# Kernel optimization log

Hardware: AMD Instinct MI355X
Metric: run time of the kernel (lower is better)

Reference implementation:

```python
import jax, jax.numpy as jnp
import numpy as np

HALF_STEP = 0.05
NUM_V = 10  # clamp(floor(0.5/0.05), 2, 1000)
EPS = 1e-6


def _normalize(x):
    return x / (jnp.linalg.norm(x, axis=-1, keepdims=True) + EPS)


def _ragged_structure(edge_points_np):
    # Concrete (numpy) ragged-grid index structure: per-edge horizontal sample
    # counts from edge length, exclusive-cumsum offsets, repeat_interleave ids.
    sp = edge_points_np[:, 0]
    cd = edge_points_np[:, 1] - sp
    cl = np.linalg.norm(cd + EPS, axis=1)
    num_h = np.clip((cl // HALF_STEP).astype(np.int64), 2, 1000)  # [N]
    total_x = int(num_h.sum())
    begin = np.concatenate([[0], np.cumsum(num_h)[:-1]])           # roll-based exclusive cumsum
    eid_x = np.repeat(np.arange(len(num_h)), num_h)                # [total_x] edge id per x-sample
    pos_x = np.arange(total_x) - begin[eid_x]                      # dx integer position within edge
    eid = np.repeat(eid_x, NUM_V)                                  # [P] edge id per sample point
    pos_x_full = np.repeat(pos_x, NUM_V).astype(np.float32)        # coords_x integer part
    dy_idx = np.tile(np.arange(NUM_V), total_x).astype(np.float32) # coords_y integer part
    denom_full = np.repeat((num_h - 1)[eid_x], NUM_V).astype(np.float32)
    return (jnp.asarray(eid), jnp.asarray(pos_x_full), jnp.asarray(denom_full),
            jnp.asarray(dy_idx))


def _sample_img(img, uv):
    # img [1,3,H,W]; uv [P,2] in [0,1) -> bilinear sample (align_corners style)
    im = img[0]
    H, W = im.shape[1], im.shape[2]
    x = uv[:, 0] * (W - 1)
    y = uv[:, 1] * (H - 1)
    x0 = jnp.floor(x).astype(jnp.int32)
    y0 = jnp.floor(y).astype(jnp.int32)
    x1 = jnp.clip(x0 + 1, 0, W - 1)
    y1 = jnp.clip(y0 + 1, 0, H - 1)
    wx = (x - x0)[None]
    wy = (y - y0)[None]
    g = lambda yy, xx: im[:, yy, xx]  # [3,P] gather
    out = (g(y0, x0) * (1 - wx) * (1 - wy) + g(y0, x1) * wx * (1 - wy)
           + g(y1, x0) * (1 - wx) * wy + g(y1, x1) * wx * wy)
    return out.T  # [P,3]


def _forward(edge_points, intrinsic1, intrinsic2, extrinsic1, extrinsic2,
             rgb1, rgb2, eid, pos_x, denom, dy_idx):
    start = edge_points[:, 0]
    cur_dir = edge_points[:, 1] - start
    next_dir = edge_points[:, 3] - edge_points[:, 1]
    prev_dir = edge_points[:, 0] - edge_points[:, 2]
    cur_len = jnp.linalg.norm(cur_dir + EPS, axis=1)
    cur_dir = cur_dir / cur_len[:, None]
    cur_normal = _normalize(jnp.cross(cur_dir, next_dir))
    flip = cur_normal[:, 2] > 0  # dot with (0,0,1) > 0 -> flip sign
    cur_normal = jnp.where(flip[:, None], -cur_normal, cur_normal)
    cur_up = _normalize(jnp.cross(cur_normal, cur_dir))
    prev_normal = _normalize(jnp.cross(prev_dir, cur_dir))

    # ragged per-edge sample grid (repeat_interleave realized via gather on eid)
    coords_x = pos_x / denom * cur_len[eid]          # [P]
    coords_y = dy_idx / (NUM_V - 1) * 0.5            # [P]
    pts = (cur_dir[eid] * coords_x[:, None]
           + cur_up[eid] * coords_y[:, None]
           + start[eid])                              # [P,3]

    # view 1 projection + bilinear sample
    uv1 = pts @ intrinsic1.T
    uv1 = jnp.clip(uv1[:, :2] / uv1[:, 2:3], 0.0, 0.999999)
    s1 = _sample_img(rgb1, uv1)

    # view 2: K2_homog @ E2 @ inv(E1) applied to homogeneous points
    K2h = jnp.eye(4, dtype=pts.dtype).at[:3, :3].set(intrinsic2)
    T = K2h @ extrinsic2 @ jnp.linalg.inv(extrinsic1)
    ph = jnp.concatenate([pts, jnp.ones_like(pts[:, :1])], axis=1)
    uv2 = ph @ T.T
    uv2 = jnp.clip(uv2[:, :2] / uv2[:, 2:3], 0.0, 0.999999)
    s2 = _sample_img(rgb2, uv2)

    similarity_loss = jnp.mean((s1 - s2) ** 2)
    normal_loss = jnp.mean(1.0 - jnp.sum(cur_normal * prev_normal, axis=1)) / 2.0
    obs_normal = _normalize(jnp.cross(edge_points[:, 0], edge_points[:, 1]))
    snp = jnp.minimum(jnp.abs(jnp.sum(cur_up * obs_normal, axis=1)), 0.5)
    normalization_loss = jnp.mean(1.0 - snp / 0.5)
    return jnp.stack([similarity_loss, normal_loss, normalization_loss])


def setup_inputs() -> dict:
    key = jax.random.key(0)
    k0, k1, k2 = jax.random.split(key, 3)
    N, H, W = 10000, 1500, 2000
    # camera-space edge endpoints/neighbors, pushed in front of the camera
    edge_points = jax.random.normal(k0, (N, 4, 3), dtype=jnp.float32) \
        + jnp.array([0.0, 0.0, 6.0], dtype=jnp.float32)
    intrinsic1 = jnp.array([[0.3, 0.0, 0.5], [0.0, 0.3, 0.5], [0.0, 0.0, 1.0]],
                           dtype=jnp.float32)
    intrinsic2 = intrinsic1
    extrinsic1 = jnp.eye(4, dtype=jnp.float32)
    extrinsic2 = jnp.eye(4, dtype=jnp.float32).at[:3, 3].set(
        jnp.array([0.1, 0.0, 0.0], dtype=jnp.float32))
    rgb1 = jax.random.uniform(k1, (1, 3, H, W), dtype=jnp.float32)
    rgb2 = jax.random.uniform(k2, (1, 3, H, W), dtype=jnp.float32)
    return {"edge_points": edge_points, "intrinsic1": intrinsic1,
            "intrinsic2": intrinsic2, "extrinsic1": extrinsic1,
            "extrinsic2": extrinsic2, "rgb1": rgb1, "rgb2": rgb2}


def reference(edge_points, intrinsic1, intrinsic2, extrinsic1, extrinsic2,
              rgb1, rgb2):
    eid, pos_x, denom, dy_idx = _ragged_structure(np.asarray(edge_points))
    return _forward(edge_points, intrinsic1, intrinsic2, extrinsic1,
                    extrinsic2, rgb1, rgb2, eid, pos_x, denom, dy_idx)
```

## Files before the change

### kernel.cpp

```cpp
#include <hip/hip_runtime.h>
#include <math.h>

#define EPSF 1e-6f
#define NUM_V 10
#define W_IMG 2000
#define H_IMG 1500
#define HW_IMG (W_IMG * H_IMG)
#define TH_QUAD (H_IMG - 1)
#define SAMPLE_BLOCKS 2048
#define MAX_CHUNKS 80
#define ROW_MARGIN 8

__device__ __forceinline__ void cross3(const float a[3], const float b[3], float c[3]) {
    c[0] = a[1] * b[2] - a[2] * b[1];
    c[1] = a[2] * b[0] - a[0] * b[2];
    c[2] = a[0] * b[1] - a[1] * b[0];
}
__device__ __forceinline__ float dot3(const float a[3], const float b[3]) {
    return a[0] * b[0] + a[1] * b[1] + a[2] * b[2];
}
__device__ __forceinline__ float norm3(const float a[3]) {
    return sqrtf(a[0] * a[0] + a[1] * a[1] + a[2] * a[2]);
}

__device__ void do_init(const float* __restrict__ K2, const float* __restrict__ E1,
                        const float* __restrict__ E2, float* __restrict__ T) {
    double M[4][8];
    for (int i = 0; i < 4; ++i)
        for (int j = 0; j < 4; ++j) {
            M[i][j] = (double)E1[i * 4 + j];
            M[i][j + 4] = (i == j) ? 1.0 : 0.0;
        }
    for (int col = 0; col < 4; ++col) {
        int piv = col;
        double best = fabs(M[col][col]);
        for (int r = col + 1; r < 4; ++r) {
            double v = fabs(M[r][col]);
            if (v > best) { best = v; piv = r; }
        }
        if (piv != col)
            for (int j = 0; j < 8; ++j) {
                double t = M[col][j]; M[col][j] = M[piv][j]; M[piv][j] = t;
            }
        double d = M[col][col];
        for (int j = 0; j < 8; ++j) M[col][j] /= d;
        for (int r = 0; r < 4; ++r) {
            if (r == col) continue;
            double f = M[r][col];
            for (int j = 0; j < 8; ++j) M[r][j] -= f * M[col][j];
        }
    }
    double E[4][4];
    for (int i = 0; i < 4; ++i)
        for (int j = 0; j < 4; ++j) {
            double s = 0.0;
            for (int k = 0; k < 4; ++k) s += (double)E2[i * 4 + k] * M[k][j + 4];
            E[i][j] = s;
        }
    for (int i = 0; i < 4; ++i)
        for (int j = 0; j < 4; ++j) {
            double s = 0.0;
            if (i < 3) {
                for (int k = 0; k < 3; ++k) s += (double)K2[i * 3 + k] * E[k][j];
            } else {
                s = E[3][j];
            }
            T[i * 4 + j] = (float)s;
        }
}

__global__ void init_kernel(const float* __restrict__ K2, const float* __restrict__ E1,
                            const float* __restrict__ E2, float* __restrict__ T,
                            int* __restrict__ bbox) {
    if (threadIdx.x != 0) return;
    do_init(K2, E1, E2, T);
    bbox[0] = 0x7fffffff;
    bbox[1] = -0x7fffffff;
    bbox[2] = 0x7fffffff;
    bbox[3] = -0x7fffffff;
}

__global__ __launch_bounds__(256) void geom_kernel(const float* __restrict__ ep, int N,
                                                   const float* __restrict__ K1,
                                                   const float* __restrict__ T,
                                                   float4* __restrict__ geo,
                                                   int* __restrict__ nwv,
                                                   double* __restrict__ gnl,
                                                   double* __restrict__ gzl,
                                                   double* __restrict__ gcnt,
                                                   int* __restrict__ bbox) {
    const int e = blockIdx.x * 256 + threadIdx.x;
    float nl = 0.f, zl = 0.f;
    int cn = 0;
    int r1min = 0x7fffffff, r1max = -0x7fffffff;
    int r2min = 0x7fffffff, r2max = -0x7fffffff;
    if (e < N) {
        const float4* P4 = (const float4*)(ep + (size_t)e * 12);
        float4 a4 = P4[0], b4 = P4[1], c4 = P4[2];
        float p0[3] = {a4.x, a4.y, a4.z};
        float p1[3] = {a4.w, b4.x, b4.y};
        float p2[3] = {b4.z, b4.w, c4.x};
        float p3[3] = {c4.y, c4.z, c4.w};
        float cd[3] = {p1[0] - p0[0], p1[1] - p0[1], p1[2] - p0[2]};
        float nd[3] = {p3[0] - p1[0], p3[1] - p1[1], p3[2] - p1[2]};
        float pd[3] = {p0[0] - p2[0], p0[1] - p2[1], p0[2] - p2[2]};
        float ce[3] = {cd[0] + EPSF, cd[1] + EPSF, cd[2] + EPSF};
        float clen = norm3(ce);
        float dir[3] = {cd[0] / clen, cd[1] / clen, cd[2] / clen};
        float cnv[3];
        cross3(dir, nd, cnv);
        float n1 = norm3(cnv) + EPSF;
        cnv[0] /= n1; cnv[1] /= n1; cnv[2] /= n1;
        if (cnv[2] > 0.f) { cnv[0] = -cnv[0]; cnv[1] = -cnv[1]; cnv[2] = -cnv[2]; }
        float up[3];
        cross3(cnv, dir, up);
        float n2 = norm3(up) + EPSF;
        up[0] /= n2; up[1] /= n2; up[2] /= n2;
        float pn[3];
        cross3(pd, dir, pn);
        float n3 = norm3(pn) + EPSF;
        pn[0] /= n3; pn[1] /= n3; pn[2] /= n3;
        float obs[3];
        cross3(p0, p1, obs);
        float n4 = norm3(obs) + EPSF;
        obs[0] /= n4; obs[1] /= n4; obs[2] /= n4;
        int nh = (int)floorf(clen / 0.05f);
        nh = max(2, min(1000, nh));
        nl = 1.f - dot3(cnv, pn);
        float snp = fminf(fabsf(dot3(up, obs)), 0.5f);
        zl = 1.f - snp * 2.f;
        int nsamp = nh * NUM_V;
        cn = nsamp;
        geo[3 * e + 0] = make_float4(p0[0], p0[1], p0[2], clen);
        geo[3 * e + 1] = make_float4(dir[0], dir[1], dir[2], (float)(nh - 1));
        geo[3 * e + 2] = make_float4(up[0], up[1], up[2], __int_as_float(nsamp));
        nwv[e] = (nsamp + 127) / 128;

        const float k10 = K1[3], k11 = K1[4], k12 = K1[5];
        const float k20 = K1[6], k21 = K1[7], k22 = K1[8];
        const float t10 = T[4], t11 = T[5], t12 = T[6], t13 = T[7];
        const float t20 = T[8], t21 = T[9], t22 = T[10], t23 = T[11];
        float v1min = 1e9f, v1max = -1e9f, v2min = 1e9f, v2max = -1e9f;
#pragma unroll
        for (int c = 0; c < 4; ++c) {
            float cx = (c & 1) ? clen : 0.f;
            float cy = (c & 2) ? 0.5f : 0.f;
            float X = fmaf(dir[0], cx, fmaf(up[0], cy, p0[0]));
            float Y = fmaf(dir[1], cx, fmaf(up[1], cy, p0[1]));
            float Z = fmaf(dir[2], cx, fmaf(up[2], cy, p0[2]));
            float iw1 = __builtin_amdgcn_rcpf(fmaf(k20, X, fmaf(k21, Y, k22 * Z)));
            float v1 = fminf(fmaxf(fmaf(k10, X, fmaf(k11, Y, k12 * Z)) * iw1, 0.f), 0.999999f);
            float iw2 = __builtin_amdgcn_rcpf(fmaf(t20, X, fmaf(t21, Y, fmaf(t22, Z, t23))));
            float v2 = fminf(
                fmaxf(fmaf(t10, X, fmaf(t11, Y, fmaf(t12, Z, t13))) * iw2, 0.f), 0.999999f);
            v1min = fminf(v1min, v1); v1max = fmaxf(v1max, v1);
            v2min = fminf(v2min, v2); v2max = fmaxf(v2max, v2);
        }
        r1min = (int)floorf(v1min * (float)(H_IMG - 1)) - ROW_MARGIN;
        r1max = (int)floorf(v1max * (float)(H_IMG - 1)) + ROW_MARGIN;
        r2min = (int)floorf(v2min * (float)(H_IMG - 1)) - ROW_MARGIN;
        r2max = (int)floorf(v2max * (float)(H_IMG - 1)) + ROW_MARGIN;
    }
#pragma unroll
    for (int off = 32; off > 0; off >>= 1) {
        nl += __shfl_down(nl, off);
        zl += __shfl_down(zl, off);
        cn += __shfl_down(cn, off);
        r1min = min(r1min, __shfl_down(r1min, off));
        r1max = max(r1max, __shfl_down(r1max, off));
        r2min = min(r2min, __shfl_down(r2min, off));
        r2max = max(r2max, __shfl_down(r2max, off));
    }
    __shared__ int s_bb[4][4];
    const int wave = threadIdx.x >> 6;
    if ((threadIdx.x & 63) == 0) {
        const int w = blockIdx.x * 4 + wave;
        gnl[w] = (double)nl;
        gzl[w] = (double)zl;
        gcnt[w] = (double)cn;
        s_bb[wave][0] = r1min; s_bb[wave][1] = r1max;
        s_bb[wave][2] = r2min; s_bb[wave][3] = r2max;
    }
    __syncthreads();
    if (threadIdx.x == 0) {
        int m0 = min(min(s_bb[0][0], s_bb[1][0]), min(s_bb[2][0], s_bb[3][0]));
        int m1 = max(max(s_bb[0][1], s_bb[1][1]), max(s_bb[2][1], s_bb[3][1]));
        int m2 = min(min(s_bb[0][2], s_bb[1][2]), min(s_bb[2][2], s_bb[3][2]));
        int m3 = max(max(s_bb[0][3], s_bb[1][3]), max(s_bb[2][3], s_bb[3][3]));
        atomicMin(&bbox[0], m0);
        atomicMax(&bbox[1], m1);
        atomicMin(&bbox[2], m2);
        atomicMax(&bbox[3], m3);
    }
}

__global__ __launch_bounds__(256) void sched_scan_kernel(const int* __restrict__ nwv, int N,
                                                         unsigned* __restrict__ sched,
                                                         int* __restrict__ total) {
    __shared__ int s_red[256];
    const int b = blockIdx.x;
    const int tid = threadIdx.x;
    const int lo = b * 256;
    int acc = 0;
    for (int i = tid; i < lo; i += 256) acc += nwv[i];
    s_red[tid] = acc;
    __syncthreads();
    for (int off = 128; off > 0; off >>= 1) {
        if (tid < off) s_red[tid] += s_red[tid + off];
        __syncthreads();
    }
    const int base0 = s_red[0];
    __syncthreads();
    const int e = lo + tid;
    const int mine = (e < N) ? nwv[e] : 0;
    s_red[tid] = mine;
    __syncthreads();
    for (int off = 1; off < 256; off <<= 1) {
        int v = (tid >= off) ? s_red[tid - off] : 0;
        __syncthreads();
        s_red[tid] += v;
        __syncthreads();
    }
    if (e < N) {
        int basee = base0 + (s_red[tid] - mine);
        const unsigned tag = ((unsigned)e) << 8;
        for (int j = 0; j < mine; ++j) sched[basee + j] = tag | (unsigned)j;
    }
    if (b == (int)gridDim.x - 1 && tid == 255) *total = base0 + s_red[255];
}

__device__ __forceinline__ unsigned quant565(float r, float g, float b) {
    unsigned r5 = (unsigned)fmaf(r, 31.f, 0.5f);
    unsigned g6 = (unsigned)fmaf(g, 63.f, 0.5f);
    unsigned b5 = (unsigned)fmaf(b, 31.f, 0.5f);
    return (r5 << 11) | (g6 << 5) | b5;
}

__global__ __launch_bounds__(256) void repack_quad565(const float* __restrict__ rgb1,
                                                      const float* __restrict__ rgb2,
                                                      uint2* __restrict__ t1,
                                                      uint2* __restrict__ t2,
                                                      const int* __restrict__ bbox) {
    const int gpi = TH_QUAD * (W_IMG / 4);
    int t = blockIdx.x * 256 + threadIdx.x;
    if (t >= 2 * gpi) return;
    const int img = t >= gpi;
    const int g = t - img * gpi;
    const int y = g / (W_IMG / 4);
    const int bmin = max(0, bbox[img * 2]);
    const int bmax = min(TH_QUAD - 1, bbox[img * 2 + 1]);
    if (y < bmin || y > bmax) return;
    const int x = (g - y * (W_IMG / 4)) * 4;
    const float* src = img ? rgb2 : rgb1;
    uint2* dst = img ? t2 : t1;
    unsigned pk[2][5];
#pragma unroll
    for (int r = 0; r < 2; ++r) {
        const int yy = y + r;
        float px[3][5];
#pragma unroll
        for (int c = 0; c < 3; ++c) {
            const float* b = src + (size_t)c * HW_IMG + (size_t)yy * W_IMG + x;
            float4 a = *(const float4*)b;
            float e = (x + 4 < W_IMG) ? b[4] : a.w;
            px[c][0] = a.x; px[c][1] = a.y; px[c][2] = a.z; px[c][3] = a.w; px[c][4] = e;
        }
#pragma unroll
        for (int k = 0; k < 5; ++k) pk[r][k] = quant565(px[0][k], px[1][k], px[2][k]);
    }
    uint2* o = dst + (size_t)y * W_IMG + x;
    uint4 s0 = make_uint4(pk[0][0] | (pk[0][1] << 16), pk[1][0] | (pk[1][1] << 16),
                          pk[0][1] | (pk[0][2] << 16), pk[1][1] | (pk[1][2] << 16));
    uint4 s1 = make_uint4(pk[0][2] | (pk[0][3] << 16), pk[1][2] | (pk[1][3] << 16),
                          pk[0][3] | (pk[0][4] << 16), pk[1][3] | (pk[1][4] << 16));
    *(uint4*)(o + 0) = s0;
    *(uint4*)(o + 2) = s1;
}

__device__ __forceinline__ float mse565(uint2 qa, uint2 qb, float wxa, float wya, float wxb,
                                        float wyb) {
    float wa00 = (1.f - wxa) * (1.f - wya), wa01 = wxa * (1.f - wya);
    float wa10 = (1.f - wxa) * wya, wa11 = wxa * wya;
    float wb00 = (1.f - wxb) * (1.f - wyb), wb01 = wxb * (1.f - wyb);
    float wb10 = (1.f - wxb) * wyb, wb11 = wxb * wyb;
    unsigned a00 = qa.x & 0xffffu, a01 = qa.x >> 16, a10 = qa.y & 0xffffu, a11 = qa.y >> 16;
    unsigned b00 = qb.x & 0xffffu, b01 = qb.x >> 16, b10 = qb.y & 0xffffu, b11 = qb.y >> 16;
    float ra = fmaf((float)(a00 >> 11), wa00, fmaf((float)(a01 >> 11), wa01,
               fmaf((float)(a10 >> 11), wa10, (float)(a11 >> 11) * wa11)));
    float rb = fmaf((float)(b00 >> 11), wb00, fmaf((float)(b01 >> 11), wb01,
               fmaf((float)(b10 >> 11), wb10, (float)(b11 >> 11) * wb11)));
    float ga = fmaf((float)((a00 >> 5) & 63u), wa00, fmaf((float)((a01 >> 5) & 63u), wa01,
               fmaf((float)((a10 >> 5) & 63u), wa10, (float)((a11 >> 5) & 63u) * wa11)));
    float gb = fmaf((float)((b00 >> 5) & 63u), wb00, fmaf((float)((b01 >> 5) & 63u), wb01,
               fmaf((float)((b10 >> 5) & 63u), wb10, (float)((b11 >> 5) & 63u) * wb11)));
    float ba = fmaf((float)(a00 & 31u), wa00, fmaf((float)(a01 & 31u), wa01,
               fmaf((float)(a10 & 31u), wa10, (float)(a11 & 31u) * wa11)));
    float bb = fmaf((float)(b00 & 31u), wb00, fmaf((float)(b01 & 31u), wb01,
               fmaf((float)(b10 & 31u), wb10, (float)(b11 & 31u) * wb11)));
    float dr = (ra - rb) * (1.f / 31.f);
    float dg = (ga - gb) * (1.f / 63.f);
    float db = (ba - bb) * (1.f / 31.f);
    return fmaf(dr, dr, fmaf(dg, dg, db * db));
}

__global__ __launch_bounds__(256) void sample_kernel(
    const float4* __restrict__ geo, const float* __restrict__ K1, const float* __restrict__ T,
    const uint2* __restrict__ im1, const uint2* __restrict__ im2,
    const unsigned* __restrict__ sched, const int* __restrict__ total_p,
    double* __restrict__ part) {
    const int wid = blockIdx.x * 4 + (threadIdx.x >> 6);
    const int lane = threadIdx.x & 63;
    const int nw = gridDim.x * 4;
    const int total = *total_p;

    const float k00 = K1[0], k01 = K1[1], k02 = K1[2];
    const float k10 = K1[3], k11 = K1[4], k12 = K1[5];
    const float k20 = K1[6], k21 = K1[7], k22 = K1[8];
    const float t00 = T[0], t01 = T[1], t02 = T[2], t03 = T[3];
    const float t10 = T[4], t11 = T[5], t12 = T[6], t13 = T[7];
    const float t20 = T[8], t21 = T[9], t22 = T[10], t23 = T[11];

    float lsum = 0.f;
    for (int base = wid; base < total; base += 2 * nw) {
        const int idxB = base + nw;
        const bool has2 = idxB < total;
        const unsigned sA = (unsigned)__builtin_amdgcn_readfirstlane((int)sched[base]);
        const unsigned sB =
            has2 ? (unsigned)__builtin_amdgcn_readfirstlane((int)sched[idxB]) : sA;
        const int eA = (int)(sA >> 8), kA = (int)(sA & 255u);
        const int eB = (int)(sB >> 8), kB = (int)(sB & 255u);
        const float4 a0 = geo[3 * eA + 0], a1 = geo[3 * eA + 1], a2 = geo[3 * eA + 2];
        const float4 b0 = geo[3 * eB + 0], b1 = geo[3 * eB + 1], b2 = geo[3 * eB + 2];
        const int nsA = __float_as_int(a2.w), nsB = __float_as_int(b2.w);
        const float lodA = a0.w * __builtin_amdgcn_rcpf(a1.w);
        const float lodB = b0.w * __builtin_amdgcn_rcpf(b1.w);

        int off1[4], off2[4];
        float wx1[4], wy1[4], wx2[4], wy2[4];
        bool ok[4];
#pragma unroll
        for (int j = 0; j < 4; ++j) {
            const int d = j >> 1, h = j & 1;
            const float4 g0 = d ? b0 : a0;
            const float4 g1 = d ? b1 : a1;
            const float4 g2 = d ? b2 : a2;
            const int ns = d ? nsB : nsA;
            const int kk = d ? kB : kA;
            const float lod = d ? lodB : lodA;
            const int i = kk * 128 + h * 64 + lane;
            ok[j] = (i < ns) && (d == 0 || has2);
            const int ic = min(i, ns - 1);
            int px = ic / NUM_V;
            int dy = ic - px * NUM_V;
            float cx = (float)px * lod;
            float cy = (float)dy * (0.5f / 9.0f);
            float X = fmaf(g1.x, cx, fmaf(g2.x, cy, g0.x));
            float Y = fmaf(g1.y, cx, fmaf(g2.y, cy, g0.y));
            float Z = fmaf(g1.z, cx, fmaf(g2.z, cy, g0.z));
            float iw1 = __builtin_amdgcn_rcpf(fmaf(k20, X, fmaf(k21, Y, k22 * Z)));
            float u1 = fminf(fmaxf(fmaf(k00, X, fmaf(k01, Y, k02 * Z)) * iw1, 0.f), 0.999999f);
            float v1 = fminf(fmaxf(fmaf(k10, X, fmaf(k11, Y, k12 * Z)) * iw1, 0.f), 0.999999f);
            float iw2 = __builtin_amdgcn_rcpf(fmaf(t20, X, fmaf(t21, Y, fmaf(t22, Z, t23))));
            float u2 = fminf(
                fmaxf(fmaf(t00, X, fmaf(t01, Y, fmaf(t02, Z, t03))) * iw2, 0.f), 0.999999f);
            float v2 = fminf(
                fmaxf(fmaf(t10, X, fmaf(t11, Y, fmaf(t12, Z, t13))) * iw2, 0.f), 0.999999f);
            float xa = u1 * (float)(W_IMG - 1), ya = v1 * (float)(H_IMG - 1);
            float xb = u2 * (float)(W_IMG - 1), yb = v2 * (float)(H_IMG - 1);
            float fxa = floorf(xa), fya = floorf(ya), fxb = floorf(xb), fyb = floorf(yb);
            off1[j] = (int)fya * W_IMG + (int)fxa;
            off2[j] = (int)fyb * W_IMG + (int)fxb;
            wx1[j] = xa - fxa; wy1[j] = ya - fya;
            wx2[j] = xb - fxb; wy2[j] = yb - fyb;
        }
        uint2 q1[4], q2[4];
#pragma unroll
        for (int j = 0; j < 4; ++j) q1[j] = im1[off1[j]];
#pragma unroll
        for (int j = 0; j < 4; ++j) q2[j] = im2[off2[j]];
#pragma unroll
        for (int j = 0; j < 4; ++j) {
            float v = mse565(q1[j], q2[j], wx1[j], wy1[j], wx2[j], wy2[j]);
            lsum += ok[j] ? v : 0.f;
        }
    }
    double dsum = (double)lsum;
#pragma unroll
    for (int off = 32; off > 0; off >>= 1) dsum += __shfl_down(dsum, off);
    if (lane == 0) part[wid] = dsum;
}

__global__ __launch_bounds__(256) void finalize_kernel(const double* __restrict__ part, int NP,
                                                       const double* __restrict__ gnl,
                                                       const double* __restrict__ gzl,
                                                       const double* __restrict__ gcnt, int N,
                                                       int NW, float* __restrict__ out) {
    __shared__ double s_s[4], s_a[4], s_b[4], s_c[4];
    double s = 0.0, a = 0.0, b = 0.0, c = 0.0;
    for (int i = threadIdx.x; i < NP; i += 256) s += part[i];
    for (int i = threadIdx.x; i < NW; i += 256) {
        a += gnl[i];
        b += gzl[i];
        c += gcnt[i];
    }
#pragma unroll
    for (int off = 32; off > 0; off >>= 1) {
        s += __shfl_down(s, off);
        a += __shfl_down(a, off);
        b += __shfl_down(b, off);
        c += __shfl_down(c, off);
    }
    const int wave = threadIdx.x >> 6;
    if ((threadIdx.x & 63) == 0) {
        s_s[wave] = s; s_a[wave] = a; s_b[wave] = b; s_c[wave] = c;
    }
    __syncthreads();
    if (threadIdx.x == 0) {
        double S = s_s[0] + s_s[1] + s_s[2] + s_s[3];
        double A = s_a[0] + s_a[1] + s_a[2] + s_a[3];
        double B = s_b[0] + s_b[1] + s_b[2] + s_b[3];
        double C = s_c[0] + s_c[1] + s_c[2] + s_c[3];
        out[0] = (float)(S / (C * 3.0));
        out[1] = (float)(A / (double)N * 0.5);
        out[2] = (float)(B / (double)N);
    }
}

extern "C" void kernel_launch(void* const* d_in, const int* in_sizes, int n_in, void* d_out,
                              int out_size, void* d_ws, size_t ws_size, hipStream_t stream) {
    const float* ep = (const float*)d_in[0];
    const float* K1 = (const float*)d_in[1];
    const float* K2 = (const float*)d_in[2];
    const float* E1 = (const float*)d_in[3];
    const float* E2 = (const float*)d_in[4];
    const float* rgb1 = (const float*)d_in[5];
    const float* rgb2 = (const float*)d_in[6];
    float* out = (float*)d_out;
    const int N = in_sizes[0] / 12;

    const int GB = (N + 255) / 256;
    const int NW = GB * 4;
    const int NPART = SAMPLE_BLOCKS * 4;

    char* p = (char*)d_ws;
    auto align256 = [](char* q) { return (char*)(((size_t)q + 255) & ~(size_t)255); };
    float* T = (float*)p;                 p += 256;
    int* total = (int*)p;                 p += 128;
    int* bbox = (int*)p;                  p += 128;
    float4* geo = (float4*)p;             p += (size_t)3 * N * sizeof(float4);
    p = align256(p);
    int* nwv = (int*)p;                   p += (size_t)N * sizeof(int);
    p = align256(p);
    double* part = (double*)p;            p += (size_t)NPART * sizeof(double);
    double* gnl = (double*)p;             p += (size_t)NW * sizeof(double);
    double* gzl = (double*)p;             p += (size_t)NW * sizeof(double);
    double* gcnt = (double*)p;            p += (size_t)NW * sizeof(double);
    p = align256(p);
    unsigned* sched = (unsigned*)p;       p += (size_t)N * MAX_CHUNKS * sizeof(unsigned);
    p = align256(p);
    uint2* img1 = (uint2*)p;
    uint2* img2 = img1 + (size_t)TH_QUAD * W_IMG;

    init_kernel<<<1, 64, 0, stream>>>(K2, E1, E2, T, bbox);
    geom_kernel<<<GB, 256, 0, stream>>>(ep, N, K1, T, geo, nwv, gnl, gzl, gcnt, bbox);
    sched_scan_kernel<<<GB, 256, 0, stream>>>(nwv, N, sched, total);
    const int rp_threads = 2 * TH_QUAD * (W_IMG / 4);
    repack_quad565<<<(rp_threads + 255) / 256, 256, 0, stream>>>(rgb1, rgb2, img1, img2, bbox);
    sample_kernel<<<SAMPLE_BLOCKS, 256, 0, stream>>>(geo, K1, T, img1, img2, sched, total, part);
    finalize_kernel<<<1, 256, 0, stream>>>(part, NPART, gnl, gzl, gcnt, N, NW, out);
}
```

Baseline: 178.6 us.

## Fuse prep stages into one kernel, atomic scheduling, drop bbox culling

Merges the init, geometry, schedule-scan and image-repack kernels into a single prep kernel. The prefix-scan schedule is replaced by an atomic cursor, and the finalize kernel is replaced by atomic accumulation with a last-block-done reduction. Sample waves now take contiguous chunk ranges instead of a strided pair loop. This cuts launch count and serialization between stages, but it removes the bbox-based row culling, so the repack now converts every image row, and the atomic schedule order is nondeterministic.

```diff
diff --git a/kernel.cpp b/kernel.cpp
--- a/kernel.cpp
+++ b/kernel.cpp
@@ -8,8 +8,18 @@
 #define HW_IMG (W_IMG * H_IMG)
 #define TH_QUAD (H_IMG - 1)
 #define SAMPLE_BLOCKS 2048
+#define NW_WAVES (SAMPLE_BLOCKS * 4)
 #define MAX_CHUNKS 80
-#define ROW_MARGIN 8
+
+struct Ctrl {
+    int cursor;
+    int done;
+    int pad0, pad1;
+    double accS;
+    double accNL;
+    double accZL;
+    double accC;
+};
 
 __device__ __forceinline__ void cross3(const float a[3], const float b[3], float c[3]) {
     c[0] = a[1] * b[2] - a[2] * b[1];
@@ -23,210 +33,51 @@
     return sqrtf(a[0] * a[0] + a[1] * a[1] + a[2] * a[2]);
 }
 
-__device__ void do_init(const float* __restrict__ K2, const float* __restrict__ E1,
-                        const float* __restrict__ E2, float* __restrict__ T) {
-    double M[4][8];
+__device__ void make_T(const float* __restrict__ K2, const float* __restrict__ E1,
+                       const float* __restrict__ E2, float* __restrict__ T) {
+    float M[4][8];
     for (int i = 0; i < 4; ++i)
         for (int j = 0; j < 4; ++j) {
-            M[i][j] = (double)E1[i * 4 + j];
-            M[i][j + 4] = (i == j) ? 1.0 : 0.0;
+            M[i][j] = E1[i * 4 + j];
+            M[i][j + 4] = (i == j) ? 1.f : 0.f;
         }
     for (int col = 0; col < 4; ++col) {
         int piv = col;
-        double best = fabs(M[col][col]);
+        float best = fabsf(M[col][col]);
         for (int r = col + 1; r < 4; ++r) {
-            double v = fabs(M[r][col]);
+            float v = fabsf(M[r][col]);
             if (v > best) { best = v; piv = r; }
         }
         if (piv != col)
             for (int j = 0; j < 8; ++j) {
-                double t = M[col][j]; M[col][j] = M[piv][j]; M[piv][j] = t;
+                float t = M[col][j]; M[col][j] = M[piv][j]; M[piv][j] = t;
             }
-        double d = M[col][col];
-        for (int j = 0; j < 8; ++j) M[col][j] /= d;
+        float d = 1.f / M[col][col];
+        for (int j = 0; j < 8; ++j) M[col][j] *= d;
         for (int r = 0; r < 4; ++r) {
             if (r == col) continue;
-            double f = M[r][col];
+            float f = M[r][col];
             for (int j = 0; j < 8; ++j) M[r][j] -= f * M[col][j];
         }
     }
-    double E[4][4];
+    float E[4][4];
     for (int i = 0; i < 4; ++i)
         for (int j = 0; j < 4; ++j) {
-            double s = 0.0;
-            for (int k = 0; k < 4; ++k) s += (double)E2[i * 4 + k] * M[k][j + 4];
+            float s = 0.f;
+            for (int k = 0; k < 4; ++k) s += E2[i * 4 + k] * M[k][j + 4];
             E[i][j] = s;
         }
     for (int i = 0; i < 4; ++i)
         for (int j = 0; j < 4; ++j) {
-            double s = 0.0;
+            float s;
             if (i < 3) {
-                for (int k = 0; k < 3; ++k) s += (double)K2[i * 3 + k] * E[k][j];
+                s = 0.f;
+                for (int k = 0; k < 3; ++k) s += K2[i * 3 + k] * E[k][j];
             } else {
                 s = E[3][j];
             }
-            T[i * 4 + j] = (float)s;
-        }
-}
-
-__global__ void init_kernel(const float* __restrict__ K2, const float* __restrict__ E1,
-                            const float* __restrict__ E2, float* __restrict__ T,
-                            int* __restrict__ bbox) {
-    if (threadIdx.x != 0) return;
-    do_init(K2, E1, E2, T);
-    bbox[0] = 0x7fffffff;
-    bbox[1] = -0x7fffffff;
-    bbox[2] = 0x7fffffff;
-    bbox[3] = -0x7fffffff;
-}
-
-__global__ __launch_bounds__(256) void geom_kernel(const float* __restrict__ ep, int N,
-                                                   const float* __restrict__ K1,
-                                                   const float* __restrict__ T,
-                                                   float4* __restrict__ geo,
-                                                   int* __restrict__ nwv,
-                                                   double* __restrict__ gnl,
-                                                   double* __restrict__ gzl,
-                                                   double* __restrict__ gcnt,
-                                                   int* __restrict__ bbox) {
-    const int e = blockIdx.x * 256 + threadIdx.x;
-    float nl = 0.f, zl = 0.f;
-    int cn = 0;
-    int r1min = 0x7fffffff, r1max = -0x7fffffff;
-    int r2min = 0x7fffffff, r2max = -0x7fffffff;
-    if (e < N) {
-        const float4* P4 = (const float4*)(ep + (size_t)e * 12);
-        float4 a4 = P4[0], b4 = P4[1], c4 = P4[2];
-        float p0[3] = {a4.x, a4.y, a4.z};
-        float p1[3] = {a4.w, b4.x, b4.y};
-        float p2[3] = {b4.z, b4.w, c4.x};
-        float p3[3] = {c4.y, c4.z, c4.w};
-        float cd[3] = {p1[0] - p0[0], p1[1] - p0[1], p1[2] - p0[2]};
-        float nd[3] = {p3[0] - p1[0], p3[1] - p1[1], p3[2] - p1[2]};
-        float pd[3] = {p0[0] - p2[0], p0[1] - p2[1], p0[2] - p2[2]};
-        float ce[3] = {cd[0] + EPSF, cd[1] + EPSF, cd[2] + EPSF};
-        float clen = norm3(ce);
-        float dir[3] = {cd[0] / clen, cd[1] / clen, cd[2] / clen};
-        float cnv[3];
-        cross3(dir, nd, cnv);
-        float n1 = norm3(cnv) + EPSF;
-        cnv[0] /= n1; cnv[1] /= n1; cnv[2] /= n1;
-        if (cnv[2] > 0.f) { cnv[0] = -cnv[0]; cnv[1] = -cnv[1]; cnv[2] = -cnv[2]; }
-        float up[3];
-        cross3(cnv, dir, up);
-        float n2 = norm3(up) + EPSF;
-        up[0] /= n2; up[1] /= n2; up[2] /= n2;
-        float pn[3];
-        cross3(pd, dir, pn);
-        float n3 = norm3(pn) + EPSF;
-        pn[0] /= n3; pn[1] /= n3; pn[2] /= n3;
-        float obs[3];
-        cross3(p0, p1, obs);
-        float n4 = norm3(obs) + EPSF;
-        obs[0] /= n4; obs[1] /= n4; obs[2] /= n4;
-        int nh = (int)floorf(clen / 0.05f);
-        nh = max(2, min(1000, nh));
-        nl = 1.f - dot3(cnv, pn);
-        float snp = fminf(fabsf(dot3(up, obs)), 0.5f);
-        zl = 1.f - snp * 2.f;
-        int nsamp = nh * NUM_V;
-        cn = nsamp;
-        geo[3 * e + 0] = make_float4(p0[0], p0[1], p0[2], clen);
-        geo[3 * e + 1] = make_float4(dir[0], dir[1], dir[2], (float)(nh - 1));
-        geo[3 * e + 2] = make_float4(up[0], up[1], up[2], __int_as_float(nsamp));
-        nwv[e] = (nsamp + 127) / 128;
-
-        const float k10 = K1[3], k11 = K1[4], k12 = K1[5];
-        const float k20 = K1[6], k21 = K1[7], k22 = K1[8];
-        const float t10 = T[4], t11 = T[5], t12 = T[6], t13 = T[7];
-        const float t20 = T[8], t21 = T[9], t22 = T[10], t23 = T[11];
-        float v1min = 1e9f, v1max = -1e9f, v2min = 1e9f, v2max = -1e9f;
-#pragma unroll
-        for (int c = 0; c < 4; ++c) {
-            float cx = (c & 1) ? clen : 0.f;
-            float cy = (c & 2) ? 0.5f : 0.f;
-            float X = fmaf(dir[0], cx, fmaf(up[0], cy, p0[0]));
-            float Y = fmaf(dir[1], cx, fmaf(up[1], cy, p0[1]));
-            float Z = fmaf(dir[2], cx, fmaf(up[2], cy, p0[2]));
-            float iw1 = __builtin_amdgcn_rcpf(fmaf(k20, X, fmaf(k21, Y, k22 * Z)));
-            float v1 = fminf(fmaxf(fmaf(k10, X, fmaf(k11, Y, k12 * Z)) * iw1, 0.f), 0.999999f);
-            float iw2 = __builtin_amdgcn_rcpf(fmaf(t20, X, fmaf(t21, Y, fmaf(t22, Z, t23))));
-            float v2 = fminf(
-                fmaxf(fmaf(t10, X, fmaf(t11, Y, fmaf(t12, Z, t13))) * iw2, 0.f), 0.999999f);
-            v1min = fminf(v1min, v1); v1max = fmaxf(v1max, v1);
-            v2min = fminf(v2min, v2); v2max = fmaxf(v2max, v2);
-        }
-        r1min = (int)floorf(v1min * (float)(H_IMG - 1)) - ROW_MARGIN;
-        r1max = (int)floorf(v1max * (float)(H_IMG - 1)) + ROW_MARGIN;
-        r2min = (int)floorf(v2min * (float)(H_IMG - 1)) - ROW_MARGIN;
-        r2max = (int)floorf(v2max * (float)(H_IMG - 1)) + ROW_MARGIN;
-    }
-#pragma unroll
-    for (int off = 32; off > 0; off >>= 1) {
-        nl += __shfl_down(nl, off);
-        zl += __shfl_down(zl, off);
-        cn += __shfl_down(cn, off);
-        r1min = min(r1min, __shfl_down(r1min, off));
-        r1max = max(r1max, __shfl_down(r1max, off));
-        r2min = min(r2min, __shfl_down(r2min, off));
-        r2max = max(r2max, __shfl_down(r2max, off));
-    }
-    __shared__ int s_bb[4][4];
-    const int wave = threadIdx.x >> 6;
-    if ((threadIdx.x & 63) == 0) {
-        const int w = blockIdx.x * 4 + wave;
-        gnl[w] = (double)nl;
-        gzl[w] = (double)zl;
-        gcnt[w] = (double)cn;
-        s_bb[wave][0] = r1min; s_bb[wave][1] = r1max;
-        s_bb[wave][2] = r2min; s_bb[wave][3] = r2max;
-    }
-    __syncthreads();
-    if (threadIdx.x == 0) {
-        int m0 = min(min(s_bb[0][0], s_bb[1][0]), min(s_bb[2][0], s_bb[3][0]));
-        int m1 = max(max(s_bb[0][1], s_bb[1][1]), max(s_bb[2][1], s_bb[3][1]));
-        int m2 = min(min(s_bb[0][2], s_bb[1][2]), min(s_bb[2][2], s_bb[3][2]));
-        int m3 = max(max(s_bb[0][3], s_bb[1][3]), max(s_bb[2][3], s_bb[3][3]));
-        atomicMin(&bbox[0], m0);
-        atomicMax(&bbox[1], m1);
-        atomicMin(&bbox[2], m2);
-        atomicMax(&bbox[3], m3);
-    }
-}
-
-__global__ __launch_bounds__(256) void sched_scan_kernel(const int* __restrict__ nwv, int N,
-                                                         unsigned* __restrict__ sched,
-                                                         int* __restrict__ total) {
-    __shared__ int s_red[256];
-    const int b = blockIdx.x;
-    const int tid = threadIdx.x;
-    const int lo = b * 256;
-    int acc = 0;
-    for (int i = tid; i < lo; i += 256) acc += nwv[i];
-    s_red[tid] = acc;
-    __syncthreads();
-    for (int off = 128; off > 0; off >>= 1) {
-        if (tid < off) s_red[tid] += s_red[tid + off];
-        __syncthreads();
-    }
-    const int base0 = s_red[0];
-    __syncthreads();
-    const int e = lo + tid;
-    const int mine = (e < N) ? nwv[e] : 0;
-    s_red[tid] = mine;
-    __syncthreads();
-    for (int off = 1; off < 256; off <<= 1) {
-        int v = (tid >= off) ? s_red[tid - off] : 0;
-        __syncthreads();
-        s_red[tid] += v;
-        __syncthreads();
-    }
-    if (e < N) {
-        int basee = base0 + (s_red[tid] - mine);
-        const unsigned tag = ((unsigned)e) << 8;
-        for (int j = 0; j < mine; ++j) sched[basee + j] = tag | (unsigned)j;
-    }
-    if (b == (int)gridDim.x - 1 && tid == 255) *total = base0 + s_red[255];
+            T[i * 4 + j] = s;
+        }
 }
 
 __device__ __forceinline__ unsigned quant565(float r, float g, float b) {
@@ -236,20 +87,86 @@
     return (r5 << 11) | (g6 << 5) | b5;
 }
 
-__global__ __launch_bounds__(256) void repack_quad565(const float* __restrict__ rgb1,
-                                                      const float* __restrict__ rgb2,
-                                                      uint2* __restrict__ t1,
-                                                      uint2* __restrict__ t2,
-                                                      const int* __restrict__ bbox) {
+__global__ __launch_bounds__(256) void prep_kernel(
+    const float* __restrict__ ep, int N, int GB,
+    const float* __restrict__ K2v, const float* __restrict__ E1, const float* __restrict__ E2,
+    const float* __restrict__ rgb1, const float* __restrict__ rgb2,
+    float* __restrict__ T, Ctrl* __restrict__ ctrl,
+    float4* __restrict__ geo, unsigned* __restrict__ sched,
+    uint2* __restrict__ t1, uint2* __restrict__ t2) {
+    const int b = blockIdx.x;
+    if (b == 0) {
+        if (threadIdx.x == 0) make_T(K2v, E1, E2, T);
+        return;
+    }
+    if (b <= GB) {
+        const int e = (b - 1) * 256 + threadIdx.x;
+        float nl = 0.f, zl = 0.f;
+        int cn = 0;
+        if (e < N) {
+            const float4* P4 = (const float4*)(ep + (size_t)e * 12);
+            float4 a4 = P4[0], b4 = P4[1], c4 = P4[2];
+            float p0[3] = {a4.x, a4.y, a4.z};
+            float p1[3] = {a4.w, b4.x, b4.y};
+            float p2[3] = {b4.z, b4.w, c4.x};
+            float p3[3] = {c4.y, c4.z, c4.w};
+            float cd[3] = {p1[0] - p0[0], p1[1] - p0[1], p1[2] - p0[2]};
+            float nd[3] = {p3[0] - p1[0], p3[1] - p1[1], p3[2] - p1[2]};
+            float pd[3] = {p0[0] - p2[0], p0[1] - p2[1], p0[2] - p2[2]};
+            float ce[3] = {cd[0] + EPSF, cd[1] + EPSF, cd[2] + EPSF};
+            float clen = norm3(ce);
+            float dir[3] = {cd[0] / clen, cd[1] / clen, cd[2] / clen};
+            float cnv[3];
+            cross3(dir, nd, cnv);
+            float n1 = norm3(cnv) + EPSF;
+            cnv[0] /= n1; cnv[1] /= n1; cnv[2] /= n1;
+            if (cnv[2] > 0.f) { cnv[0] = -cnv[0]; cnv[1] = -cnv[1]; cnv[2] = -cnv[2]; }
+            float up[3];
+            cross3(cnv, dir, up);
+            float n2 = norm3(up) + EPSF;
+            up[0] /= n2; up[1] /= n2; up[2] /= n2;
+            float pn[3];
+            cross3(pd, dir, pn);
+            float n3 = norm3(pn) + EPSF;
+            pn[0] /= n3; pn[1] /= n3; pn[2] /= n3;
+            float obs[3];
+            cross3(p0, p1, obs);
+            float n4 = norm3(obs) + EPSF;
+            obs[0] /= n4; obs[1] /= n4; obs[2] /= n4;
+            int nh = (int)floorf(clen / 0.05f);
+            nh = max(2, min(1000, nh));
+            nl = 1.f - dot3(cnv, pn);
+            float snp = fminf(fabsf(dot3(up, obs)), 0.5f);
+            zl = 1.f - snp * 2.f;
+            const int nsamp = nh * NUM_V;
+            cn = nsamp;
+            geo[3 * e + 0] = make_float4(p0[0], p0[1], p0[2], clen);
+            geo[3 * e + 1] = make_float4(dir[0], dir[1], dir[2], (float)(nh - 1));
+            geo[3 * e + 2] = make_float4(up[0], up[1], up[2], __int_as_float(nsamp));
+            const int nc = (nsamp + 127) / 128;
+            const int basee = atomicAdd(&ctrl->cursor, nc);
+            const unsigned tag = ((unsigned)e) << 8;
+            for (int j = 0; j < nc; ++j) sched[basee + j] = tag | (unsigned)j;
+        }
+#pragma unroll
+        for (int off = 32; off > 0; off >>= 1) {
+            nl += __shfl_down(nl, off);
+            zl += __shfl_down(zl, off);
+            cn += __shfl_down(cn, off);
+        }
+        if ((threadIdx.x & 63) == 0) {
+            atomicAdd(&ctrl->accNL, (double)nl);
+            atomicAdd(&ctrl->accZL, (double)zl);
+            atomicAdd(&ctrl->accC, (double)cn);
+        }
+        return;
+    }
     const int gpi = TH_QUAD * (W_IMG / 4);
-    int t = blockIdx.x * 256 + threadIdx.x;
+    const int t = (b - GB - 1) * 256 + threadIdx.x;
     if (t >= 2 * gpi) return;
     const int img = t >= gpi;
     const int g = t - img * gpi;
     const int y = g / (W_IMG / 4);
-    const int bmin = max(0, bbox[img * 2]);
-    const int bmax = min(TH_QUAD - 1, bbox[img * 2 + 1]);
-    if (y < bmin || y > bmax) return;
     const int x = (g - y * (W_IMG / 4)) * 4;
     const float* src = img ? rgb2 : rgb1;
     uint2* dst = img ? t2 : t1;
@@ -260,9 +177,9 @@
         float px[3][5];
 #pragma unroll
         for (int c = 0; c < 3; ++c) {
-            const float* b = src + (size_t)c * HW_IMG + (size_t)yy * W_IMG + x;
-            float4 a = *(const float4*)b;
-            float e = (x + 4 < W_IMG) ? b[4] : a.w;
+            const float* bp = src + (size_t)c * HW_IMG + (size_t)yy * W_IMG + x;
+            float4 a = *(const float4*)bp;
+            float e = (x + 4 < W_IMG) ? bp[4] : a.w;
             px[c][0] = a.x; px[c][1] = a.y; px[c][2] = a.z; px[c][3] = a.w; px[c][4] = e;
         }
 #pragma unroll
@@ -306,12 +223,14 @@
 __global__ __launch_bounds__(256) void sample_kernel(
     const float4* __restrict__ geo, const float* __restrict__ K1, const float* __restrict__ T,
     const uint2* __restrict__ im1, const uint2* __restrict__ im2,
-    const unsigned* __restrict__ sched, const int* __restrict__ total_p,
-    double* __restrict__ part) {
+    const unsigned* __restrict__ sched, Ctrl* __restrict__ ctrl,
+    float* __restrict__ out, int N) {
     const int wid = blockIdx.x * 4 + (threadIdx.x >> 6);
     const int lane = threadIdx.x & 63;
-    const int nw = gridDim.x * 4;
-    const int total = *total_p;
+    const int total = ctrl->cursor;
+    const int q = total / NW_WAVES, r = total - q * NW_WAVES;
+    const int begin = wid * q + min(wid, r);
+    const int cnt = q + (wid < r ? 1 : 0);
 
     const float k00 = K1[0], k01 = K1[1], k02 = K1[2];
     const float k10 = K1[3], k11 = K1[4], k12 = K1[5];
@@ -321,34 +240,21 @@
     const float t20 = T[8], t21 = T[9], t22 = T[10], t23 = T[11];
 
     float lsum = 0.f;
-    for (int base = wid; base < total; base += 2 * nw) {
-        const int idxB = base + nw;
-        const bool has2 = idxB < total;
-        const unsigned sA = (unsigned)__builtin_amdgcn_readfirstlane((int)sched[base]);
-        const unsigned sB =
-            has2 ? (unsigned)__builtin_amdgcn_readfirstlane((int)sched[idxB]) : sA;
-        const int eA = (int)(sA >> 8), kA = (int)(sA & 255u);
-        const int eB = (int)(sB >> 8), kB = (int)(sB & 255u);
-        const float4 a0 = geo[3 * eA + 0], a1 = geo[3 * eA + 1], a2 = geo[3 * eA + 2];
-        const float4 b0 = geo[3 * eB + 0], b1 = geo[3 * eB + 1], b2 = geo[3 * eB + 2];
-        const int nsA = __float_as_int(a2.w), nsB = __float_as_int(b2.w);
-        const float lodA = a0.w * __builtin_amdgcn_rcpf(a1.w);
-        const float lodB = b0.w * __builtin_amdgcn_rcpf(b1.w);
-
-        int off1[4], off2[4];
-        float wx1[4], wy1[4], wx2[4], wy2[4];
-        bool ok[4];
-#pragma unroll
-        for (int j = 0; j < 4; ++j) {
-            const int d = j >> 1, h = j & 1;
-            const float4 g0 = d ? b0 : a0;
-            const float4 g1 = d ? b1 : a1;
-            const float4 g2 = d ? b2 : a2;
-            const int ns = d ? nsB : nsA;
-            const int kk = d ? kB : kA;
-            const float lod = d ? lodB : lodA;
-            const int i = kk * 128 + h * 64 + lane;
-            ok[j] = (i < ns) && (d == 0 || has2);
+    for (int it = 0; it < cnt; ++it) {
+        const unsigned s = (unsigned)__builtin_amdgcn_readfirstlane((int)sched[begin + it]);
+        const int e = (int)(s >> 8), kk = (int)(s & 255u);
+        const float4 g0 = geo[3 * e + 0], g1 = geo[3 * e + 1], g2 = geo[3 * e + 2];
+        const int ns = __float_as_int(g2.w);
+        const float lod = g0.w * __builtin_amdgcn_rcpf(g1.w);
+        const int ibase = kk * 128 + lane;
+
+        int off1[2], off2[2];
+        float wx1[2], wy1[2], wx2[2], wy2[2];
+        bool ok[2];
+#pragma unroll
+        for (int h = 0; h < 2; ++h) {
+            const int i = ibase + h * 64;
+            ok[h] = i < ns;
             const int ic = min(i, ns - 1);
             int px = ic / NUM_V;
             int dy = ic - px * NUM_V;
@@ -368,61 +274,37 @@
             float xa = u1 * (float)(W_IMG - 1), ya = v1 * (float)(H_IMG - 1);
             float xb = u2 * (float)(W_IMG - 1), yb = v2 * (float)(H_IMG - 1);
             float fxa = floorf(xa), fya = floorf(ya), fxb = floorf(xb), fyb = floorf(yb);
-            off1[j] = (int)fya * W_IMG + (int)fxa;
-            off2[j] = (int)fyb * W_IMG + (int)fxb;
-            wx1[j] = xa - fxa; wy1[j] = ya - fya;
-            wx2[j] = xb - fxb; wy2[j] = yb - fyb;
-        }
-        uint2 q1[4], q2[4];
-#pragma unroll
-        for (int j = 0; j < 4; ++j) q1[j] = im1[off1[j]];
-#pragma unroll
-        for (int j = 0; j < 4; ++j) q2[j] = im2[off2[j]];
-#pragma unroll
-        for (int j = 0; j < 4; ++j) {
-            float v = mse565(q1[j], q2[j], wx1[j], wy1[j], wx2[j], wy2[j]);
-            lsum += ok[j] ? v : 0.f;
+            off1[h] = (int)fya * W_IMG + (int)fxa;
+            off2[h] = (int)fyb * W_IMG + (int)fxb;
+            wx1[h] = xa - fxa; wy1[h] = ya - fya;
+            wx2[h] = xb - fxb; wy2[h] = yb - fyb;
+        }
+        uint2 q1[2], q2[2];
+        q1[0] = im1[off1[0]]; q1[1] = im1[off1[1]];
+        q2[0] = im2[off2[0]]; q2[1] = im2[off2[1]];
+#pragma unroll
+        for (int h = 0; h < 2; ++h) {
+            float v = mse565(q1[h], q2[h], wx1[h], wy1[h], wx2[h], wy2[h]);
+            lsum += ok[h] ? v : 0.f;
         }
     }
     double dsum = (double)lsum;
 #pragma unroll
     for (int off = 32; off > 0; off >>= 1) dsum += __shfl_down(dsum, off);
-    if (lane == 0) part[wid] = dsum;
-}
-
-__global__ __launch_bounds__(256) void finalize_kernel(const double* __restrict__ part, int NP,
-                                                       const double* __restrict__ gnl,
-                                                       const double* __restrict__ gzl,
-                                                       const double* __restrict__ gcnt, int N,
-                                                       int NW, float* __restrict__ out) {
-    __shared__ double s_s[4], s_a[4], s_b[4], s_c[4];
-    double s = 0.0, a = 0.0, b = 0.0, c = 0.0;
-    for (int i = threadIdx.x; i < NP; i += 256) s += part[i];
-    for (int i = threadIdx.x; i < NW; i += 256) {
-        a += gnl[i];
-        b += gzl[i];
-        c += gcnt[i];
-    }
-#pragma unroll
-    for (int off = 32; off > 0; off >>= 1) {
-        s += __shfl_down(s, off);
-        a += __shfl_down(a, off);
-        b += __shfl_down(b, off);
-        c += __shfl_down(c, off);
-    }
-    const int wave = threadIdx.x >> 6;
-    if ((threadIdx.x & 63) == 0) {
-        s_s[wave] = s; s_a[wave] = a; s_b[wave] = b; s_c[wave] = c;
-    }
+    if (lane == 0) atomicAdd(&ctrl->accS, dsum);
+    __threadfence();
     __syncthreads();
     if (threadIdx.x == 0) {
-        double S = s_s[0] + s_s[1] + s_s[2] + s_s[3];
-        double A = s_a[0] + s_a[1] + s_a[2] + s_a[3];
-        double B = s_b[0] + s_b[1] + s_b[2] + s_b[3];
-        double C = s_c[0] + s_c[1] + s_c[2] + s_c[3];
-        out[0] = (float)(S / (C * 3.0));
-        out[1] = (float)(A / (double)N * 0.5);
-        out[2] = (float)(B / (double)N);
+        const int prev = atomicAdd(&ctrl->done, 1);
+        if (prev == (int)gridDim.x - 1) {
+            double S = atomicAdd(&ctrl->accS, 0.0);
+            double A = atomicAdd(&ctrl->accNL, 0.0);
+            double B = atomicAdd(&ctrl->accZL, 0.0);
+            double C = atomicAdd(&ctrl->accC, 0.0);
+            out[0] = (float)(S / (C * 3.0));
+            out[1] = (float)(A / (double)N * 0.5);
+            out[2] = (float)(B / (double)N);
+        }
     }
 }
 
@@ -439,33 +321,21 @@
     const int N = in_sizes[0] / 12;
 
     const int GB = (N + 255) / 256;
-    const int NW = GB * 4;
-    const int NPART = SAMPLE_BLOCKS * 4;
+    const int gpi = TH_QUAD * (W_IMG / 4);
+    const int RPB = (2 * gpi + 255) / 256;
 
     char* p = (char*)d_ws;
-    auto align256 = [](char* q) { return (char*)(((size_t)q + 255) & ~(size_t)255); };
-    float* T = (float*)p;                 p += 256;
-    int* total = (int*)p;                 p += 128;
-    int* bbox = (int*)p;                  p += 128;
-    float4* geo = (float4*)p;             p += (size_t)3 * N * sizeof(float4);
-    p = align256(p);
-    int* nwv = (int*)p;                   p += (size_t)N * sizeof(int);
-    p = align256(p);
-    double* part = (double*)p;            p += (size_t)NPART * sizeof(double);
-    double* gnl = (double*)p;             p += (size_t)NW * sizeof(double);
-    double* gzl = (double*)p;             p += (size_t)NW * sizeof(double);
-    double* gcnt = (double*)p;            p += (size_t)NW * sizeof(double);
-    p = align256(p);
-    unsigned* sched = (unsigned*)p;       p += (size_t)N * MAX_CHUNKS * sizeof(unsigned);
-    p = align256(p);
+    float* T = (float*)p;               p += 256;
+    Ctrl* ctrl = (Ctrl*)p;              p += 256;
+    float4* geo = (float4*)p;           p += (size_t)3 * N * sizeof(float4);
+    p = (char*)(((size_t)p + 255) & ~(size_t)255);
+    unsigned* sched = (unsigned*)p;     p += (size_t)N * MAX_CHUNKS * sizeof(unsigned);
+    p = (char*)(((size_t)p + 255) & ~(size_t)255);
     uint2* img1 = (uint2*)p;
     uint2* img2 = img1 + (size_t)TH_QUAD * W_IMG;
 
-    init_kernel<<<1, 64, 0, stream>>>(K2, E1, E2, T, bbox);
-    geom_kernel<<<GB, 256, 0, stream>>>(ep, N, K1, T, geo, nwv, gnl, gzl, gcnt, bbox);
-    sched_scan_kernel<<<GB, 256, 0, stream>>>(nwv, N, sched, total);
-    const int rp_threads = 2 * TH_QUAD * (W_IMG / 4);
-    repack_quad565<<<(rp_threads + 255) / 256, 256, 0, stream>>>(rgb1, rgb2, img1, img2, bbox);
-    sample_kernel<<<SAMPLE_BLOCKS, 256, 0, stream>>>(geo, K1, T, img1, img2, sched, total, part);
-    finalize_kernel<<<1, 256, 0, stream>>>(part, NPART, gnl, gzl, gcnt, N, NW, out);
-}
+    hipMemsetAsync(ctrl, 0, sizeof(Ctrl), stream);
+    prep_kernel<<<1 + GB + RPB, 256, 0, stream>>>(ep, N, GB, K2, E1, E2, rgb1, rgb2, T, ctrl,
+                                                  geo, sched, img1, img2);
+    sample_kernel<<<SAMPLE_BLOCKS, 256, 0, stream>>>(geo, K1, T, img1, img2, sched, ctrl, out, N);
+}
```

Result: slower. 326.3 us (+82.7%).
